# Kernel tuning notes

Measured on AMD Instinct MI355X. Metric: run time of the kernel, lower is better.

## Reference

```python
import jax, jax.numpy as jnp
import numpy as np


def _lstm_layer(x, h0, c0, W_ih, W_hh, b_ih, b_hh):
    # x: [B,T,D], h0/c0: [B,H], W_ih: [4H,D], W_hh: [4H,H]
    # Precompute input contribution for all timesteps (one big GEMM).
    xg = jnp.einsum('btd,gd->btg', x, W_ih) + (b_ih + b_hh)  # [B,T,4H]

    def step(carry, xg_t):
        h, c = carry
        g = xg_t + h @ W_hh.T  # [B,4H]
        i, f, gg, o = jnp.split(g, 4, axis=-1)  # torch gate order: i,f,g,o
        i = jax.nn.sigmoid(i)
        f = jax.nn.sigmoid(f)
        gg = jnp.tanh(gg)
        o = jax.nn.sigmoid(o)
        c = f * c + i * gg
        h = o * jnp.tanh(c)
        return (h, c), h

    (hT, cT), hs = jax.lax.scan(step, (h0, c0), jnp.swapaxes(xg, 0, 1))
    return jnp.swapaxes(hs, 0, 1), hT, cT  # [B,T,H], [B,H], [B,H]


def setup_inputs() -> dict:
    key = jax.random.key(0)
    ks = jax.random.split(key, 20)
    B, T, D, H, O = 32, 2048, 64, 256, 32
    s = 0.05
    return {
        'inputs': jax.random.normal(ks[0], (B, T, D), jnp.float32),
        'h0': jax.random.normal(ks[1], (2, B, H), jnp.float32) * s,
        'c0': jax.random.normal(ks[2], (2, B, H), jnp.float32) * s,
        'W_ih0': jax.random.normal(ks[3], (4 * H, D), jnp.float32) * s,
        'W_hh0': jax.random.normal(ks[4], (4 * H, H), jnp.float32) * s,
        'b_ih0': jax.random.normal(ks[5], (4 * H,), jnp.float32) * s,
        'b_hh0': jax.random.normal(ks[6], (4 * H,), jnp.float32) * s,
        'W_ih1': jax.random.normal(ks[7], (4 * H, H), jnp.float32) * s,
        'W_hh1': jax.random.normal(ks[8], (4 * H, H), jnp.float32) * s,
        'b_ih1': jax.random.normal(ks[9], (4 * H,), jnp.float32) * s,
        'b_hh1': jax.random.normal(ks[10], (4 * H,), jnp.float32) * s,
        'W_d0': jax.random.normal(ks[11], (H, H), jnp.float32) * s,
        'b_d0': jax.random.normal(ks[12], (H,), jnp.float32) * s,
        'W_d1': jax.random.normal(ks[13], (H, H), jnp.float32) * s,
        'b_d1': jax.random.normal(ks[14], (H,), jnp.float32) * s,
        'W_out': jax.random.normal(ks[15], (O, H), jnp.float32) * s,
        'b_out': jax.random.normal(ks[16], (O,), jnp.float32) * s,
    }


def reference(inputs, h0, c0, W_ih0, W_hh0, b_ih0, b_hh0,
              W_ih1, W_hh1, b_ih1, b_hh1,
              W_d0, b_d0, W_d1, b_d1, W_out, b_out):
    # Stacked 2-layer LSTM (batch_first) matching torch nn.LSTM.
    y0, h_0, c_0 = _lstm_layer(inputs, h0[0], c0[0], W_ih0, W_hh0, b_ih0, b_hh0)
    y1, h_1, c_1 = _lstm_layer(y0, h0[1], c0[1], W_ih1, W_hh1, b_ih1, b_hh1)
    h_n = jnp.stack([h_0, h_1], axis=0)
    c_n = jnp.stack([c_0, c_1], axis=0)
    # Dense head: two Linear+ReLU, then output Linear.
    d = jax.nn.relu(jnp.einsum('bth,oh->bto', y1, W_d0) + b_d0)
    d = jax.nn.relu(jnp.einsum('bth,oh->bto', d, W_d1) + b_d1)
    out = jnp.einsum('bth,oh->bto', d, W_out) + b_out
    return out, h_n, c_n
```

## Files before the change

kernel.cpp:

```cpp
#include <hip/hip_runtime.h>
#include <hip/hip_bf16.h>
#include <cstddef>
#include <cstdint>

#define BB 32
#define TT 2048
#define DD 64
#define HH 256
#define OO 32

#define OUT_ELEMS (BB*TT*OO)
#define HN_OFF OUT_ELEMS
#define CN_OFF (HN_OFF + 2*BB*HH)

#define O_XBF   ((size_t)0)
#define O_H0    (O_XBF + (size_t)8388608)
#define O_XH1   (O_H0 + (size_t)33570816)
#define O_WC0   (O_XH1 + (size_t)67141632)
#define O_WC1   (O_WC0 + 655360)
#define O_B0    (O_WC1 + 1048576)
#define O_B1    (O_B0 + 4096)
#define O_WD0T  (O_B1 + 4096)
#define O_WD1T  (O_WD0T + 262144)
#define O_WOUT  (O_WD1T + 262144)
#define O_DONE0 (O_WOUT + 32768)
#define O_DONE1 (O_DONE0 + 8192)

typedef short short8 __attribute__((ext_vector_type(8)));
typedef float f32x4 __attribute__((ext_vector_type(4)));

__device__ __forceinline__ float sigm_(float x){ return 1.0f/(1.0f+__expf(-x)); }
__device__ __forceinline__ float tanhf_(float x){
    float xc = fminf(fmaxf(x, -15.0f), 15.0f);
    float e = __expf(2.0f*xc);
    return (e-1.0f)/(e+1.0f);
}
__device__ __forceinline__ unsigned short f2bf(float f){
    __hip_bfloat16 h = __float2bfloat16(f);
    return *reinterpret_cast<unsigned short*>(&h);
}

__global__ void prep_kernel(const float* __restrict__ x, const float* __restrict__ h0,
    const float* __restrict__ Wih0, const float* __restrict__ Whh0,
    const float* __restrict__ bih0, const float* __restrict__ bhh0,
    const float* __restrict__ Wih1, const float* __restrict__ Whh1,
    const float* __restrict__ bih1, const float* __restrict__ bhh1,
    const float* __restrict__ Wd0, const float* __restrict__ Wd1,
    const float* __restrict__ Wout, char* __restrict__ ws)
{
    int i = blockIdx.x*256 + threadIdx.x;
    if (i < 4194304) { ((unsigned short*)(ws+O_XBF))[i] = f2bf(x[i]); return; }
    i -= 4194304;
    if (i < 327680) {
        int g = i/320, k = i - g*320;
        float v = (k < 64) ? Wih0[g*64 + k] : Whh0[g*256 + (k-64)];
        ((unsigned short*)(ws+O_WC0))[i] = f2bf(v); return;
    }
    i -= 327680;
    if (i < 524288) {
        int g = i >> 9, k = i & 511;
        float v = (k < 256) ? Wih1[g*256 + k] : Whh1[g*256 + (k-256)];
        ((unsigned short*)(ws+O_WC1))[i] = f2bf(v); return;
    }
    i -= 524288;
    if (i < 1024) { ((float*)(ws+O_B0))[i] = bih0[i] + bhh0[i]; return; }
    i -= 1024;
    if (i < 1024) { ((float*)(ws+O_B1))[i] = bih1[i] + bhh1[i]; return; }
    i -= 1024;
    if (i < 8192) { ((unsigned short*)(ws+O_H0))[i] = f2bf(h0[i]); return; }
    i -= 8192;
    if (i < 8192) {
        int b = i >> 8, h = i & 255;
        ((unsigned short*)(ws+O_XH1))[b*512 + 256 + h] = f2bf(h0[8192 + i]); return;
    }
    i -= 8192;
    if (i < 65536) { int o = i & 255, h = i >> 8; ((float*)(ws+O_WD0T))[i] = Wd0[o*256 + h]; return; }
    i -= 65536;
    if (i < 65536) { int o = i & 255, h = i >> 8; ((float*)(ws+O_WD1T))[i] = Wd1[o*256 + h]; return; }
    i -= 65536;
    if (i < 8192) { int o = i & 31, h = i >> 5; ((float*)(ws+O_WOUT))[i] = Wout[o*256 + h]; return; }
    i -= 8192;
    if (i < 4096) { ((int*)(ws+O_DONE0))[i] = 0; return; }
}

__device__ __forceinline__ void spin_done(int* p){
    int it = 0;
    while (__hip_atomic_load(p, __ATOMIC_RELAXED, __HIP_MEMORY_SCOPE_AGENT) < 16) {
        __builtin_amdgcn_s_sleep(2);
        if (++it > (1<<20)) break;
    }
    __builtin_amdgcn_fence(__ATOMIC_ACQUIRE, "agent");
}

template<int L>
__device__ void lstm_body(int j, int tid, char* ws,
                          const float* __restrict__ c0_in,
                          float* __restrict__ out,
                          float (*Glds)[32][17])
{
    constexpr int KK  = L ? 512 : 320;
    constexpr int NKT = KK / 32;
    const unsigned short* W   = (const unsigned short*)(ws + (L ? O_WC1 : O_WC0));
    const float* bias         = (const float*)(ws + (L ? O_B1 : O_B0));
    const unsigned short* xbf = (const unsigned short*)(ws + O_XBF);
    unsigned short* h0buf     = (unsigned short*)(ws + O_H0);
    unsigned short* xh1buf    = (unsigned short*)(ws + O_XH1);
    int* done0 = (int*)(ws + O_DONE0);
    int* done1 = (int*)(ws + O_DONE1);

    const int wv = tid >> 6, lane = tid & 63;
    const int gg = wv & 3, bh = wv >> 2;
    const int lrow = lane & 15;
    const int koff = (lane >> 4) * 8;
    const int arow = 256*gg + 16*j + lrow;
    const int fb   = bh*16 + lrow;

    short8 afr[NKT];
#pragma unroll
    for (int kk = 0; kk < NKT; ++kk)
        afr[kk] = *(const short8*)(W + (size_t)arow*KK + 32*kk + koff);

    const int ch = tid & 15;
    const int cb = tid >> 4;
    const int hg = 16*j + ch;
    float c = c0_in[(size_t)L*8192 + cb*256 + hg];
    const float b_i = bias[hg], b_f = bias[256+hg], b_g = bias[512+hg], b_o = bias[768+hg];
    float h_last = 0.0f;

    for (int t = 0; t < TT; ++t) {
        if (L == 0) { if (t > 0) spin_done(done0 + (t-1)); }
        else        { spin_done(done0 + t); if (t > 0) spin_done(done1 + (t-1)); }

        f32x4 acc = {0.f, 0.f, 0.f, 0.f};
        if (L == 0) {
            const unsigned short* xb = xbf  + ((size_t)fb*TT + t)*64 + koff;
            const unsigned short* hb = h0buf + (size_t)t*8192 + fb*256 + koff;
#pragma unroll
            for (int kk = 0; kk < 2; ++kk)
                acc = __builtin_amdgcn_mfma_f32_16x16x32_bf16(afr[kk],
                        *(const short8*)(xb + 32*kk), acc, 0, 0, 0);
#pragma unroll
            for (int kk = 0; kk < 8; ++kk)
                acc = __builtin_amdgcn_mfma_f32_16x16x32_bf16(afr[2+kk],
                        *(const short8*)(hb + 32*kk), acc, 0, 0, 0);
        } else {
            const unsigned short* xh = xh1buf + (size_t)t*16384 + fb*512 + koff;
#pragma unroll
            for (int kk = 0; kk < 16; ++kk)
                acc = __builtin_amdgcn_mfma_f32_16x16x32_bf16(afr[kk],
                        *(const short8*)(xh + 32*kk), acc, 0, 0, 0);
        }

        {
            const int n = lane & 15, m4 = (lane >> 4) * 4;
#pragma unroll
            for (int r = 0; r < 4; ++r)
                Glds[gg][bh*16 + n][m4 + r] = acc[r];
        }
        __syncthreads();

        float gi = Glds[0][cb][ch] + b_i;
        float gf = Glds[1][cb][ch] + b_f;
        float gc = Glds[2][cb][ch] + b_g;
        float go = Glds[3][cb][ch] + b_o;
        float iv = sigm_(gi), fv = sigm_(gf), gv = tanhf_(gc), ov = sigm_(go);
        c = fv*c + iv*gv;
        float hn = ov * tanhf_(c);
        h_last = hn;

        unsigned int us = f2bf(hn);
        unsigned int other = __shfl_xor(us, 1, 64);
        unsigned int word = us | (other << 16);
        if ((tid & 1) == 0) {
            if (L == 0) {
                size_t e0 = (size_t)(t+1)*8192 + (size_t)cb*256 + hg;
                __hip_atomic_store((unsigned int*)(h0buf + e0), word,
                                   __ATOMIC_RELAXED, __HIP_MEMORY_SCOPE_AGENT);
                size_t e1 = (size_t)t*16384 + (size_t)cb*512 + hg;
                __hip_atomic_store((unsigned int*)(xh1buf + e1), word,
                                   __ATOMIC_RELAXED, __HIP_MEMORY_SCOPE_AGENT);
            } else {
                size_t e2 = (size_t)(t+1)*16384 + (size_t)cb*512 + 256 + hg;
                __hip_atomic_store((unsigned int*)(xh1buf + e2), word,
                                   __ATOMIC_RELAXED, __HIP_MEMORY_SCOPE_AGENT);
            }
        }
        __syncthreads();
        if (tid == 0)
            __hip_atomic_fetch_add((L ? done1 : done0) + t, 1,
                                   __ATOMIC_RELEASE, __HIP_MEMORY_SCOPE_AGENT);
    }

    out[HN_OFF + (size_t)L*8192 + cb*256 + hg] = h_last;
    out[CN_OFF + (size_t)L*8192 + cb*256 + hg] = c;
}

__global__ __launch_bounds__(512, 1) void lstm_fused(char* ws,
                                                     const float* __restrict__ c0_in,
                                                     float* __restrict__ out)
{
    __shared__ float Glds[4][32][17];
    const int blk = blockIdx.x, tid = threadIdx.x;
    if (blk < 16) lstm_body<0>(blk,      tid, ws, c0_in, out, Glds);
    else          lstm_body<1>(blk - 16, tid, ws, c0_in, out, Glds);
}

__global__ __launch_bounds__(256) void head_kernel(const char* __restrict__ ws,
    const float* __restrict__ bd0, const float* __restrict__ bd1,
    const float* __restrict__ bout, float* __restrict__ out)
{
    const __hip_bfloat16* xh1 = (const __hip_bfloat16*)(ws + O_XH1);
    const float* Wd0T  = (const float*)(ws + O_WD0T);
    const float* Wd1T  = (const float*)(ws + O_WD1T);
    const float* WoutT = (const float*)(ws + O_WOUT);

    __shared__ float buf0[16][256];
    __shared__ float buf1[16][256];
    const int row0 = blockIdx.x * 16;
    const int tid = threadIdx.x;

#pragma unroll
    for (int i = 0; i < 16; ++i) {
        int r = row0 + i;
        int b = r >> 11, t = r & 2047;
        buf0[i][tid] = __bfloat162float(xh1[(size_t)(t+1)*16384 + b*512 + 256 + tid]);
    }
    __syncthreads();

    {
        float acc[16];
        float bv = bd0[tid];
#pragma unroll
        for (int r = 0; r < 16; ++r) acc[r] = bv;
        for (int h = 0; h < 256; ++h) {
            float w = Wd0T[h*256 + tid];
#pragma unroll
            for (int r = 0; r < 16; ++r) acc[r] += w * buf0[r][h];
        }
        __syncthreads();
#pragma unroll
        for (int r = 0; r < 16; ++r) buf1[r][tid] = fmaxf(acc[r], 0.0f);
    }
    __syncthreads();

    {
        float acc[16];
        float bv = bd1[tid];
#pragma unroll
        for (int r = 0; r < 16; ++r) acc[r] = bv;
        for (int h = 0; h < 256; ++h) {
            float w = Wd1T[h*256 + tid];
#pragma unroll
            for (int r = 0; r < 16; ++r) acc[r] += w * buf1[r][h];
        }
        __syncthreads();
#pragma unroll
        for (int r = 0; r < 16; ++r) buf0[r][tid] = fmaxf(acc[r], 0.0f);
    }
    __syncthreads();

    {
        const int o = tid & 31;
        const int rr = tid >> 5;
        float a0 = bout[o], a1 = bout[o];
        for (int h = 0; h < 256; ++h) {
            float w = WoutT[h*32 + o];
            a0 += w * buf0[rr*2 + 0][h];
            a1 += w * buf0[rr*2 + 1][h];
        }
        out[(size_t)(row0 + rr*2 + 0)*32 + o] = a0;
        out[(size_t)(row0 + rr*2 + 1)*32 + o] = a1;
    }
}

extern "C" void kernel_launch(void* const* d_in, const int* in_sizes, int n_in,
                              void* d_out, int out_size, void* d_ws, size_t ws_size,
                              hipStream_t stream) {
    const float* x    = (const float*)d_in[0];
    const float* h0   = (const float*)d_in[1];
    const float* c0   = (const float*)d_in[2];
    const float* Wih0 = (const float*)d_in[3];
    const float* Whh0 = (const float*)d_in[4];
    const float* bih0 = (const float*)d_in[5];
    const float* bhh0 = (const float*)d_in[6];
    const float* Wih1 = (const float*)d_in[7];
    const float* Whh1 = (const float*)d_in[8];
    const float* bih1 = (const float*)d_in[9];
    const float* bhh1 = (const float*)d_in[10];
    const float* Wd0  = (const float*)d_in[11];
    const float* bd0  = (const float*)d_in[12];
    const float* Wd1  = (const float*)d_in[13];
    const float* bd1  = (const float*)d_in[14];
    const float* Wout = (const float*)d_in[15];
    const float* bout = (const float*)d_in[16];

    char* ws = (char*)d_ws;
    float* out = (float*)d_out;

    prep_kernel<<<20344, 256, 0, stream>>>(x, h0, Wih0, Whh0, bih0, bhh0,
                                           Wih1, Whh1, bih1, bhh1,
                                           Wd0, Wd1, Wout, ws);
    lstm_fused<<<32, 512, 0, stream>>>(ws, c0, out);
    head_kernel<<<4096, 256, 0, stream>>>(ws, bd0, bd1, bout, out);
}
```

Baseline: 13.75 ms.

## Restructure persistent LSTM: per-wave flags, register gate exchange, fewer blocks

Cuts the persistent LSTM from 32 to 16 blocks. Each wave now computes all four gates for its hidden units using two MFMA accumulators, with weight rows permuted so the gates can be swapped through a cross-lane shuffle instead of going through LDS and __syncthreads. The per-timestep block-level counter is replaced by monotonically increasing per-wave flags that all lanes of a wave poll together, and the input x is transposed to time-major so loads stream along t. This shortens the serial per-step critical path, but each wave holds twice as many weight fragments in registers and the spin loop no longer sleeps.

```diff
diff --git a/kernel.cpp b/kernel.cpp
--- a/kernel.cpp
+++ b/kernel.cpp
@@ -8,23 +8,24 @@
 #define DD 64
 #define HH 256
 #define OO 32
+#define NBLK 8
 
 #define OUT_ELEMS (BB*TT*OO)
 #define HN_OFF OUT_ELEMS
 #define CN_OFF (HN_OFF + 2*BB*HH)
 
 #define O_XBF   ((size_t)0)
-#define O_H0    (O_XBF + (size_t)8388608)
-#define O_XH1   (O_H0 + (size_t)33570816)
-#define O_WC0   (O_XH1 + (size_t)67141632)
-#define O_WC1   (O_WC0 + 655360)
-#define O_B0    (O_WC1 + 1048576)
-#define O_B1    (O_B0 + 4096)
-#define O_WD0T  (O_B1 + 4096)
-#define O_WD1T  (O_WD0T + 262144)
-#define O_WOUT  (O_WD1T + 262144)
-#define O_DONE0 (O_WOUT + 32768)
-#define O_DONE1 (O_DONE0 + 8192)
+#define O_H0    ((size_t)8388608)
+#define O_XH1   ((size_t)41959424)
+#define O_WP0   ((size_t)109101056)
+#define O_WP1   ((size_t)109756416)
+#define O_B0    ((size_t)110804992)
+#define O_B1    ((size_t)110809088)
+#define O_WD0T  ((size_t)110813184)
+#define O_WD1T  ((size_t)111075328)
+#define O_WOUT  ((size_t)111337472)
+#define O_D0    ((size_t)111370240)
+#define O_D1    ((size_t)111378432)
 
 typedef short short8 __attribute__((ext_vector_type(8)));
 typedef float f32x4 __attribute__((ext_vector_type(4)));
@@ -38,6 +39,12 @@
 __device__ __forceinline__ unsigned short f2bf(float f){
     __hip_bfloat16 h = __float2bfloat16(f);
     return *reinterpret_cast<unsigned short*>(&h);
+}
+__device__ __forceinline__ unsigned int pack2(float a, float b){
+    return (unsigned int)f2bf(a) | ((unsigned int)f2bf(b) << 16);
+}
+__device__ __forceinline__ short8 ld8(const unsigned short* p){
+    return *reinterpret_cast<const short8*>(p);
 }
 
 __global__ void prep_kernel(const float* __restrict__ x, const float* __restrict__ h0,
@@ -49,18 +56,32 @@
     const float* __restrict__ Wout, char* __restrict__ ws)
 {
     int i = blockIdx.x*256 + threadIdx.x;
-    if (i < 4194304) { ((unsigned short*)(ws+O_XBF))[i] = f2bf(x[i]); return; }
+    if (i < 4194304) {
+        int t = i >> 11, rem = i & 2047, b = rem >> 6, d = rem & 63;
+        ((unsigned short*)(ws+O_XBF))[i] = f2bf(x[(size_t)b*131072 + t*64 + d]);
+        return;
+    }
     i -= 4194304;
     if (i < 327680) {
-        int g = i/320, k = i - g*320;
-        float v = (k < 64) ? Wih0[g*64 + k] : Whh0[g*256 + (k-64)];
-        ((unsigned short*)(ws+O_WC0))[i] = f2bf(v); return;
+        int R = i / 320, k = i - R*320;
+        int lrow = R & 15, s = (R>>4)&1, hr = (R>>5)&3, jj = R>>7;
+        int gate = 2*s + (lrow>>3);
+        int h = 32*jj + 8*hr + (lrow&7);
+        int src = 256*gate + h;
+        float v = (k < 64) ? Wih0[src*64 + k] : Whh0[src*256 + (k-64)];
+        ((unsigned short*)(ws+O_WP0))[i] = f2bf(v);
+        return;
     }
     i -= 327680;
     if (i < 524288) {
-        int g = i >> 9, k = i & 511;
-        float v = (k < 256) ? Wih1[g*256 + k] : Whh1[g*256 + (k-256)];
-        ((unsigned short*)(ws+O_WC1))[i] = f2bf(v); return;
+        int R = i >> 9, k = i & 511;
+        int lrow = R & 15, s = (R>>4)&1, hr = (R>>5)&3, jj = R>>7;
+        int gate = 2*s + (lrow>>3);
+        int h = 32*jj + 8*hr + (lrow&7);
+        int src = 256*gate + h;
+        float v = (k < 256) ? Wih1[src*256 + k] : Whh1[src*256 + (k-256)];
+        ((unsigned short*)(ws+O_WP1))[i] = f2bf(v);
+        return;
     }
     i -= 524288;
     if (i < 1024) { ((float*)(ws+O_B0))[i] = bih0[i] + bhh0[i]; return; }
@@ -71,7 +92,8 @@
     i -= 8192;
     if (i < 8192) {
         int b = i >> 8, h = i & 255;
-        ((unsigned short*)(ws+O_XH1))[b*512 + 256 + h] = f2bf(h0[8192 + i]); return;
+        ((unsigned short*)(ws+O_XH1))[b*512 + 256 + h] = f2bf(h0[8192 + i]);
+        return;
     }
     i -= 8192;
     if (i < 65536) { int o = i & 255, h = i >> 8; ((float*)(ws+O_WD0T))[i] = Wd0[o*256 + h]; return; }
@@ -80,129 +102,151 @@
     i -= 65536;
     if (i < 8192) { int o = i & 31, h = i >> 5; ((float*)(ws+O_WOUT))[i] = Wout[o*256 + h]; return; }
     i -= 8192;
-    if (i < 4096) { ((int*)(ws+O_DONE0))[i] = 0; return; }
-}
-
-__device__ __forceinline__ void spin_done(int* p){
-    int it = 0;
-    while (__hip_atomic_load(p, __ATOMIC_RELAXED, __HIP_MEMORY_SCOPE_AGENT) < 16) {
-        __builtin_amdgcn_s_sleep(2);
-        if (++it > (1<<20)) break;
-    }
-    __builtin_amdgcn_fence(__ATOMIC_ACQUIRE, "agent");
+    if (i < 4096) { ((int*)(ws+O_D0))[i] = 0; return; }
 }
 
 template<int L>
-__device__ void lstm_body(int j, int tid, char* ws,
-                          const float* __restrict__ c0_in,
-                          float* __restrict__ out,
-                          float (*Glds)[32][17])
+__device__ void lstm_body(int j, char* ws, const float* __restrict__ c0_in,
+                          float* __restrict__ out)
 {
     constexpr int KK  = L ? 512 : 320;
     constexpr int NKT = KK / 32;
-    const unsigned short* W   = (const unsigned short*)(ws + (L ? O_WC1 : O_WC0));
-    const float* bias         = (const float*)(ws + (L ? O_B1 : O_B0));
-    const unsigned short* xbf = (const unsigned short*)(ws + O_XBF);
-    unsigned short* h0buf     = (unsigned short*)(ws + O_H0);
-    unsigned short* xh1buf    = (unsigned short*)(ws + O_XH1);
-    int* done0 = (int*)(ws + O_DONE0);
-    int* done1 = (int*)(ws + O_DONE1);
-
-    const int wv = tid >> 6, lane = tid & 63;
-    const int gg = wv & 3, bh = wv >> 2;
+
+    const int tid  = threadIdx.x;
+    const int wv   = tid >> 6;
+    const int lane = tid & 63;
+    const int bh   = wv >> 2;
+    const int hr   = wv & 3;
     const int lrow = lane & 15;
-    const int koff = (lane >> 4) * 8;
-    const int arow = 256*gg + 16*j + lrow;
+    const int q    = lane >> 4;
+    const int koff = q * 8;
+    const int qe   = q & 1;
     const int fb   = bh*16 + lrow;
-
-    short8 afr[NKT];
-#pragma unroll
-    for (int kk = 0; kk < NKT; ++kk)
-        afr[kk] = *(const short8*)(W + (size_t)arow*KK + 32*kk + koff);
-
-    const int ch = tid & 15;
-    const int cb = tid >> 4;
-    const int hg = 16*j + ch;
-    float c = c0_in[(size_t)L*8192 + cb*256 + hg];
-    const float b_i = bias[hg], b_f = bias[256+hg], b_g = bias[512+hg], b_o = bias[768+hg];
-    float h_last = 0.0f;
+    const int hbase= 32*j + 8*hr + 4*qe;
+    const bool lo  = (lane < 32);
+
+    const unsigned short* Wp = (const unsigned short*)(ws + (L ? O_WP1 : O_WP0));
+    const float* bias = (const float*)(ws + (L ? O_B1 : O_B0));
+
+    const int wavebase = (j*4 + hr) * 32;
+    short8 a0[NKT], a1[NKT];
+#pragma unroll
+    for (int kk = 0; kk < NKT; ++kk) {
+        a0[kk] = ld8(Wp + (size_t)(wavebase +      lrow)*KK + kk*32 + koff);
+        a1[kk] = ld8(Wp + (size_t)(wavebase + 16 + lrow)*KK + kk*32 + koff);
+    }
+
+    float bi[4], bf_[4], bg[4], bo[4], c[4], hv[4];
+#pragma unroll
+    for (int r = 0; r < 4; ++r) {
+        int hg = hbase + r;
+        bi[r] = bias[hg];       bf_[r] = bias[256+hg];
+        bg[r] = bias[512+hg];   bo[r]  = bias[768+hg];
+        c[r]  = c0_in[(size_t)L*8192 + fb*256 + hg];
+        hv[r] = 0.f;
+    }
+
+    int* d0 = (int*)(ws + O_D0);
+    int* d1 = (int*)(ws + O_D1);
+    int* myflag = (L ? d1 : d0) + (j*8 + wv) * 32;
+    int* poll0  = d0 + lane * 32;
+    int* poll1  = d1 + lane * 32;
+
+    const unsigned short* xb = (const unsigned short*)(ws + O_XBF) + fb*64  + koff;
+    const unsigned short* hb = (const unsigned short*)(ws + O_H0)  + fb*256 + koff;
+    const unsigned short* xh = (const unsigned short*)(ws + O_XH1) + fb*512 + koff;
+
+    unsigned long long* stA;
+    unsigned long long* stB = nullptr;
+    if (L == 0) {
+        stA = (unsigned long long*)((unsigned short*)(ws + O_H0)  + (size_t)8192 + fb*256 + hbase);
+        stB = (unsigned long long*)((unsigned short*)(ws + O_XH1) + (size_t)fb*512 + hbase);
+    } else {
+        stA = (unsigned long long*)((unsigned short*)(ws + O_XH1) + (size_t)16384 + fb*512 + 256 + hbase);
+    }
 
     for (int t = 0; t < TT; ++t) {
-        if (L == 0) { if (t > 0) spin_done(done0 + (t-1)); }
-        else        { spin_done(done0 + t); if (t > 0) spin_done(done1 + (t-1)); }
-
-        f32x4 acc = {0.f, 0.f, 0.f, 0.f};
+        short8 b[NKT];
+        if (L == 0) { b[0] = ld8(xb); b[1] = ld8(xb + 32); }
+
+        {
+            const int tgt0 = (L == 0) ? t : t + 1;
+            int it = 0;
+            while (true) {
+                int v0 = __hip_atomic_load(poll0, __ATOMIC_RELAXED, __HIP_MEMORY_SCOPE_AGENT);
+                bool ok = (v0 >= tgt0);
+                if (L == 1) {
+                    int v1 = __hip_atomic_load(poll1, __ATOMIC_RELAXED, __HIP_MEMORY_SCOPE_AGENT);
+                    ok = ok && (v1 >= t);
+                }
+                if (__all(ok)) break;
+                if (++it > (1<<17)) break;
+            }
+            __builtin_amdgcn_fence(__ATOMIC_ACQUIRE, "agent");
+        }
+
         if (L == 0) {
-            const unsigned short* xb = xbf  + ((size_t)fb*TT + t)*64 + koff;
-            const unsigned short* hb = h0buf + (size_t)t*8192 + fb*256 + koff;
-#pragma unroll
-            for (int kk = 0; kk < 2; ++kk)
-                acc = __builtin_amdgcn_mfma_f32_16x16x32_bf16(afr[kk],
-                        *(const short8*)(xb + 32*kk), acc, 0, 0, 0);
-#pragma unroll
-            for (int kk = 0; kk < 8; ++kk)
-                acc = __builtin_amdgcn_mfma_f32_16x16x32_bf16(afr[2+kk],
-                        *(const short8*)(hb + 32*kk), acc, 0, 0, 0);
+#pragma unroll
+            for (int kk = 0; kk < 8; ++kk) b[2+kk] = ld8(hb + 32*kk);
         } else {
-            const unsigned short* xh = xh1buf + (size_t)t*16384 + fb*512 + koff;
-#pragma unroll
-            for (int kk = 0; kk < 16; ++kk)
-                acc = __builtin_amdgcn_mfma_f32_16x16x32_bf16(afr[kk],
-                        *(const short8*)(xh + 32*kk), acc, 0, 0, 0);
-        }
-
-        {
-            const int n = lane & 15, m4 = (lane >> 4) * 4;
-#pragma unroll
-            for (int r = 0; r < 4; ++r)
-                Glds[gg][bh*16 + n][m4 + r] = acc[r];
-        }
-        __syncthreads();
-
-        float gi = Glds[0][cb][ch] + b_i;
-        float gf = Glds[1][cb][ch] + b_f;
-        float gc = Glds[2][cb][ch] + b_g;
-        float go = Glds[3][cb][ch] + b_o;
-        float iv = sigm_(gi), fv = sigm_(gf), gv = tanhf_(gc), ov = sigm_(go);
-        c = fv*c + iv*gv;
-        float hn = ov * tanhf_(c);
-        h_last = hn;
-
-        unsigned int us = f2bf(hn);
-        unsigned int other = __shfl_xor(us, 1, 64);
-        unsigned int word = us | (other << 16);
-        if ((tid & 1) == 0) {
-            if (L == 0) {
-                size_t e0 = (size_t)(t+1)*8192 + (size_t)cb*256 + hg;
-                __hip_atomic_store((unsigned int*)(h0buf + e0), word,
-                                   __ATOMIC_RELAXED, __HIP_MEMORY_SCOPE_AGENT);
-                size_t e1 = (size_t)t*16384 + (size_t)cb*512 + hg;
-                __hip_atomic_store((unsigned int*)(xh1buf + e1), word,
-                                   __ATOMIC_RELAXED, __HIP_MEMORY_SCOPE_AGENT);
-            } else {
-                size_t e2 = (size_t)(t+1)*16384 + (size_t)cb*512 + 256 + hg;
-                __hip_atomic_store((unsigned int*)(xh1buf + e2), word,
-                                   __ATOMIC_RELAXED, __HIP_MEMORY_SCOPE_AGENT);
-            }
-        }
-        __syncthreads();
-        if (tid == 0)
-            __hip_atomic_fetch_add((L ? done1 : done0) + t, 1,
-                                   __ATOMIC_RELEASE, __HIP_MEMORY_SCOPE_AGENT);
-    }
-
-    out[HN_OFF + (size_t)L*8192 + cb*256 + hg] = h_last;
-    out[CN_OFF + (size_t)L*8192 + cb*256 + hg] = c;
-}
-
-__global__ __launch_bounds__(512, 1) void lstm_fused(char* ws,
+#pragma unroll
+            for (int kk = 0; kk < NKT; ++kk) b[kk] = ld8(xh + 32*kk);
+        }
+
+        f32x4 A0 = {0.f,0.f,0.f,0.f}, A1 = {0.f,0.f,0.f,0.f};
+#pragma unroll
+        for (int kk = 0; kk < NKT; ++kk) {
+            A0 = __builtin_amdgcn_mfma_f32_16x16x32_bf16(a0[kk], b[kk], A0, 0,0,0);
+            A1 = __builtin_amdgcn_mfma_f32_16x16x32_bf16(a1[kk], b[kk], A1, 0,0,0);
+        }
+
+#pragma unroll
+        for (int r = 0; r < 4; ++r) {
+            float x0 = A0[r], y0 = __shfl_xor(x0, 32, 64);
+            float x1 = A1[r], y1 = __shfl_xor(x1, 32, 64);
+            float gi = (lo ? x0 : y0) + bi[r];
+            float gf = (lo ? y0 : x0) + bf_[r];
+            float gg = (lo ? x1 : y1) + bg[r];
+            float go = (lo ? y1 : x1) + bo[r];
+            float iv = sigm_(gi), fv = sigm_(gf), gv = tanhf_(gg), ov = sigm_(go);
+            c[r]  = fv*c[r] + iv*gv;
+            hv[r] = ov * tanhf_(c[r]);
+        }
+
+        unsigned long long w =
+            (unsigned long long)pack2(hv[0], hv[1]) |
+            ((unsigned long long)pack2(hv[2], hv[3]) << 32);
+
+        if (L == 0) {
+            if (lo) __hip_atomic_store(stA, w, __ATOMIC_RELAXED, __HIP_MEMORY_SCOPE_AGENT);
+            else    __hip_atomic_store(stB, w, __ATOMIC_RELAXED, __HIP_MEMORY_SCOPE_AGENT);
+        } else {
+            if (lo) __hip_atomic_store(stA, w, __ATOMIC_RELAXED, __HIP_MEMORY_SCOPE_AGENT);
+        }
+
+        if (lane == 0)
+            __hip_atomic_store(myflag, t+1, __ATOMIC_RELEASE, __HIP_MEMORY_SCOPE_AGENT);
+
+        xb += 2048; hb += 8192; xh += 16384;
+        stA += (L ? 4096 : 2048);
+        if (L == 0) stB += 4096;
+    }
+
+    if (lo) {
+#pragma unroll
+        for (int r = 0; r < 4; ++r) {
+            out[HN_OFF + (size_t)L*8192 + fb*256 + hbase + r] = hv[r];
+            out[CN_OFF + (size_t)L*8192 + fb*256 + hbase + r] = c[r];
+        }
+    }
+}
+
+__global__ __launch_bounds__(512, 2) void lstm_fused(char* ws,
                                                      const float* __restrict__ c0_in,
                                                      float* __restrict__ out)
 {
-    __shared__ float Glds[4][32][17];
-    const int blk = blockIdx.x, tid = threadIdx.x;
-    if (blk < 16) lstm_body<0>(blk,      tid, ws, c0_in, out, Glds);
-    else          lstm_body<1>(blk - 16, tid, ws, c0_in, out, Glds);
+    if (blockIdx.x < NBLK) lstm_body<0>(blockIdx.x, ws, c0_in, out);
+    else                   lstm_body<1>(blockIdx.x - NBLK, ws, c0_in, out);
 }
 
 __global__ __launch_bounds__(256) void head_kernel(const char* __restrict__ ws,
@@ -300,6 +344,6 @@
     prep_kernel<<<20344, 256, 0, stream>>>(x, h0, Wih0, Whh0, bih0, bhh0,
                                            Wih1, Whh1, bih1, bhh1,
                                            Wd0, Wd1, Wout, ws);
-    lstm_fused<<<32, 512, 0, stream>>>(ws, c0, out);
+    lstm_fused<<<2*NBLK, 512, 0, stream>>>(ws, c0, out);
     head_kernel<<<4096, 256, 0, stream>>>(ws, bd0, bd1, bout, out);
 }
```

Result: slower. 21.69 ms (+57.7%).
